# Kernel tuning notes

Measured on AMD Instinct MI355X. Metric: run time of the kernel, lower is better.

Reference implementation:

```python
import jax, jax.numpy as jnp
import numpy as np

# irreps_in = irreps_out = "32x0e + 16x1o"; irreps_edge = "1x0e + 1x1o"
N_SCAL, N_VEC = 32, 16
RADIAL_EMBED, HIDDEN = 64, 64
# FullyConnectedTensorProduct instructions (uvw), v == 1 since edge mults are 1:
#  P1: 0e x 0e -> 0e (32*32)   P2: 1o x 1o -> 0e (16*32)
#  P3: 0e x 1o -> 1o (32*16)   P4: 1o x 0e -> 1o (16*16)   P5: 1o x 1o -> 1o (16*16)
SPLITS = np.cumsum([0, 32 * 32, 16 * 32, 32 * 16, 16 * 16, 16 * 16])
W_NUMEL = int(SPLITS[-1])  # 2560
SILU_NORM = 1.6790425  # e3nn normalize2mom constant for silu
# path weights: alpha = ir_out.dim / sum(num_elements over paths into same output)
PW0 = (1.0 / (32.0 + 16.0)) ** 0.5          # scalar output paths
PW1 = (3.0 / (32.0 + 16.0 + 16.0)) ** 0.5   # vector output paths
INV_SQRT3 = 3.0 ** -0.5  # wigner_3j(0,1,1)/(1,0,1)/(1,1,0) magnitude
INV_SQRT6 = 6.0 ** -0.5  # wigner_3j(1,1,1) = eps_ijk / sqrt(6)
N_NODES, N_EDGES = 8192, 65536


def radial_net(e, W0, W1, W2):
    # e3nn FullyConnectedNet: x @ (W / sqrt(fan_in)), normalized silu between layers
    h = e
    for W in (W0, W1):
        h = jax.nn.silu(h @ (W / jnp.sqrt(jnp.float32(W.shape[0])))) * SILU_NORM
    return h @ (W2 / jnp.sqrt(jnp.float32(W2.shape[0])))


def setup_inputs() -> dict:
    key = jax.random.key(0)
    ks = jax.random.split(key, 9)
    edge_index = jax.random.randint(ks[0], (2, N_EDGES), 0, N_NODES)
    node_feat = jax.random.normal(ks[1], (N_NODES, N_SCAL + 3 * N_VEC), jnp.float32)
    edge_feat = jax.random.normal(ks[2], (N_EDGES, 4), jnp.float32)
    edge_embed = jax.random.normal(ks[3], (N_EDGES, RADIAL_EMBED), jnp.float32)
    W_fc0 = jax.random.normal(ks[4], (RADIAL_EMBED, HIDDEN), jnp.float32)
    W_fc1 = jax.random.normal(ks[5], (HIDDEN, HIDDEN), jnp.float32)
    W_fc2 = jax.random.normal(ks[6], (HIDDEN, W_NUMEL), jnp.float32)
    Wsc0 = jax.random.normal(ks[7], (N_SCAL, N_SCAL), jnp.float32)
    Wsc1 = jax.random.normal(ks[8], (N_VEC, N_VEC), jnp.float32)
    return dict(edge_index=edge_index, node_feat=node_feat, edge_feat=edge_feat,
                edge_embed=edge_embed, dim_size=N_NODES,
                W_fc0=W_fc0, W_fc1=W_fc1, W_fc2=W_fc2, Wsc0=Wsc0, Wsc1=Wsc1)


def reference(edge_index, node_feat, edge_feat, edge_embed, dim_size,
              W_fc0, W_fc1, W_fc2, Wsc0, Wsc1):
    src, dst = edge_index[0], edge_index[1]
    w = radial_net(edge_embed, W_fc0, W_fc1, W_fc2)  # [E, 2560]
    W1 = w[:, SPLITS[0]:SPLITS[1]].reshape(-1, 32, 32)
    W2 = w[:, SPLITS[1]:SPLITS[2]].reshape(-1, 16, 32)
    W3 = w[:, SPLITS[2]:SPLITS[3]].reshape(-1, 32, 16)
    W4 = w[:, SPLITS[3]:SPLITS[4]].reshape(-1, 16, 16)
    W5 = w[:, SPLITS[4]:SPLITS[5]].reshape(-1, 16, 16)
    xe = node_feat[src]                                    # gather [E, 80]
    x0 = xe[:, :N_SCAL]                                    # [E, 32]
    x1 = xe[:, N_SCAL:].reshape(-1, N_VEC, 3)              # [E, 16, 3]
    y0, y1 = edge_feat[:, 0], edge_feat[:, 1:4]            # [E], [E, 3]
    # scalar outputs
    dot = jnp.einsum('eui,ei->eu', x1, y1)
    out0 = PW0 * (jnp.einsum('euw,eu,e->ew', W1, x0, y0)
                  + INV_SQRT3 * jnp.einsum('euw,eu->ew', W2, dot))
    # vector outputs ((x cross y)_k = eps_ijk x_i y_j)
    cross = jnp.cross(x1, y1[:, None, :])
    out1 = PW1 * (INV_SQRT3 * jnp.einsum('euw,eu,ek->ewk', W3, x0, y1)
                  + INV_SQRT3 * jnp.einsum('euw,euk,e->ewk', W4, x1, y0)
                  + INV_SQRT6 * jnp.einsum('euw,euk->ewk', W5, cross))
    msg = jnp.concatenate([out0, out1.reshape(-1, 3 * N_VEC)], axis=1)  # [E, 80]
    agg = jax.ops.segment_sum(msg, dst, num_segments=dim_size)          # [N, 80]
    # self-connection: e3nn o3.Linear applied per irrep, / sqrt(fan_in)
    n0 = node_feat[:, :N_SCAL]
    n1 = node_feat[:, N_SCAL:].reshape(-1, N_VEC, 3)
    sc0 = n0 @ Wsc0 / jnp.sqrt(jnp.float32(N_SCAL))
    sc1 = jnp.einsum('nui,uv->nvi', n1, Wsc1) / jnp.sqrt(jnp.float32(N_VEC))
    sc = jnp.concatenate([sc0, sc1.reshape(-1, 3 * N_VEC)], axis=1)
    return agg + sc
```

## Files before the change

kernel.cpp:

```cpp
#include <hip/hip_runtime.h>

typedef unsigned short u16;
typedef __bf16 bf16x8 __attribute__((ext_vector_type(8)));
typedef float  f32x4  __attribute__((ext_vector_type(4)));

#define NEDGES 65536
#define NNODES 8192
#define EPB 64

#define PW0f       0.14433756729740643f
#define PW1f       0.21650635094610965f
#define INV_SQRT3f 0.5773502691896258f
#define INV_SQRT6f 0.4082482904638631f
#define SILU_NORMf 1.6790425f

#define WT2_OFF 0
#define WT0_OFF 163840
#define WT1_OFF 167936
#define WS_ELEMS 172032

#define OFF_CNT   344064
#define OFF_OFS   376832
#define OFF_CUR   409856
#define OFF_ELIST 442624
#define OFF_MSG   704768
#define WS_NEED   21676288

#define HSTR 72

__device__ __forceinline__ float silu_n(float z) {
    return SILU_NORMf * z / (1.0f + __expf(-z));
}
__device__ __forceinline__ u16 f2bf(float f) {
    return __builtin_bit_cast(u16, (__bf16)f);
}
__device__ __forceinline__ float bf2f(u16 u) {
    unsigned v = ((unsigned)u) << 16;
    return __builtin_bit_cast(float, v);
}
__device__ __forceinline__ bf16x8 ld_bf8(const u16* p) {
    return *reinterpret_cast<const bf16x8*>(p);
}
__device__ __forceinline__ bf16x8 cvt_bf8(const float* p) {
    float4 a = *reinterpret_cast<const float4*>(p);
    float4 b = *reinterpret_cast<const float4*>(p + 4);
    bf16x8 r;
    r[0]=(__bf16)a.x; r[1]=(__bf16)a.y; r[2]=(__bf16)a.z; r[3]=(__bf16)a.w;
    r[4]=(__bf16)b.x; r[5]=(__bf16)b.y; r[6]=(__bf16)b.z; r[7]=(__bf16)b.w;
    return r;
}
#define MFMA16(A,B,C) __builtin_amdgcn_mfma_f32_16x16x32_bf16(A,B,C,0,0,0)

__global__ void k_zero(int* __restrict__ cnt) {
    int i = blockIdx.x * 256 + threadIdx.x;
    if (i < NNODES) cnt[i] = 0;
}

__global__ void k_prep(const float* __restrict__ Wfc0,
                       const float* __restrict__ Wfc1,
                       const float* __restrict__ Wfc2,
                       const float* __restrict__ node_feat,
                       const float* __restrict__ Wsc0,
                       const float* __restrict__ Wsc1,
                       const int*   __restrict__ eidx,
                       u16* __restrict__ ws,
                       int* __restrict__ cnt,
                       float* __restrict__ out)
{
    const int bid = blockIdx.x;
    if (bid < 672) {
        int gid = bid * 256 + threadIdx.x;
        if (gid < 163840) {
            int k = gid / 2560;
            int j = gid - k * 2560;
            float s;
            if (j < 1024)      s = PW0f;
            else if (j < 1536) s = PW0f * INV_SQRT3f;
            else if (j < 2304) s = PW1f * INV_SQRT3f;
            else               s = PW1f * INV_SQRT6f;
            ws[WT2_OFF + j * 64 + k] = f2bf(Wfc2[gid] * (0.125f * s));
        } else if (gid < WT1_OFF) {
            int i = gid - WT0_OFF;
            int k = i >> 6, n = i & 63;
            ws[WT0_OFF + n * 64 + k] = f2bf(Wfc0[i] * 0.125f);
        } else if (gid < WS_ELEMS) {
            int i = gid - WT1_OFF;
            int k = i >> 6, n = i & 63;
            ws[WT1_OFF + n * 64 + k] = f2bf(Wfc1[i] * 0.125f);
        }
    } else if (bid < 3232) {
        int gid = (bid - 672) * 256 + threadIdx.x;
        if (gid >= NNODES * 80) return;
        int n = gid / 80;
        int s = gid - n * 80;
        const float* nf = node_feat + (size_t)n * 80;
        float r;
        if (s < 32) {
            float a = 0.f;
            #pragma unroll
            for (int u = 0; u < 32; ++u) a += nf[u] * Wsc0[u * 32 + s];
            r = a * 0.17677669529663687f;
        } else {
            int v = (s - 32) / 3;
            int k = (s - 32) - v * 3;
            float a = 0.f;
            #pragma unroll
            for (int u = 0; u < 16; ++u) a += nf[32 + u * 3 + k] * Wsc1[u * 16 + v];
            r = a * 0.25f;
        }
        out[gid] = r;
    } else {
        int e = (bid - 3232) * 256 + threadIdx.x;
        if (e < NEDGES) atomicAdd(&cnt[eidx[NEDGES + e]], 1);
    }
}

__global__ __launch_bounds__(1024) void k_scan(const int* __restrict__ cnt,
                                               int* __restrict__ ofs,
                                               int* __restrict__ cur)
{
    __shared__ int ps[1024];
    const int t = threadIdx.x;
    const int base = t * 8;
    int v[8]; int s = 0;
    #pragma unroll
    for (int i = 0; i < 8; ++i) { v[i] = cnt[base + i]; s += v[i]; }
    ps[t] = s;
    __syncthreads();
    int acc = s;
    for (int off = 1; off < 1024; off <<= 1) {
        int x = (t >= off) ? ps[t - off] : 0;
        __syncthreads();
        acc += x;
        ps[t] = acc;
        __syncthreads();
    }
    int run = acc - s;
    #pragma unroll
    for (int i = 0; i < 8; ++i) { ofs[base + i] = run; cur[base + i] = run; run += v[i]; }
    if (t == 1023) ofs[NNODES] = run;
}

__global__ void k_fill(const int* __restrict__ eidx,
                       int* __restrict__ cur,
                       int* __restrict__ elist)
{
    int e = blockIdx.x * 256 + threadIdx.x;
    int d = eidx[NEDGES + e];
    int pos = atomicAdd(&cur[d], 1);
    elist[pos] = e;
}

template<int TAIL>
__global__ __launch_bounds__(256, 3) void k_main(
    const int*   __restrict__ eidx,
    const float* __restrict__ node_feat,
    const float* __restrict__ edge_feat,
    const float* __restrict__ edge_embed,
    const u16*   __restrict__ ws,
    float*       __restrict__ msgbuf,
    float*       __restrict__ out)
{
    __shared__ __align__(16) char smem[40192];
    u16*   h1S   = (u16*)(smem);
    u16*   c12S  = (u16*)(smem + 9216);
    u16*   coefB = (u16*)(smem + 15360);
    int*   dstS  = (int*)(smem + 39936);
    u16*   h0S   = (u16*)(smem + 15360);
    float* msgS  = (float*)(smem + 9216);

    const int t    = threadIdx.x;
    const int lane = t & 63;
    const int l15  = lane & 15;
    const int lq   = lane >> 4;
    const int wid  = t >> 6;
    const int role = (wid + blockIdx.x) & 3;
    const int eg0  = blockIdx.x * EPB;

    const u16* WT2 = ws + WT2_OFF;
    const u16* WT0 = ws + WT0_OFF;
    const u16* WT1 = ws + WT1_OFF;

    {
        const float* erow = edge_embed + (size_t)(eg0 + wid * 16 + l15) * 64 + 8 * lq;
        bf16x8 eB0 = cvt_bf8(erow);
        bf16x8 eB1 = cvt_bf8(erow + 32);
        #pragma unroll
        for (int ntl = 0; ntl < 4; ++ntl) {
            const u16* a = WT0 + (ntl * 16 + l15) * 64 + 8 * lq;
            bf16x8 A0 = ld_bf8(a);
            bf16x8 A1 = ld_bf8(a + 32);
            f32x4 z = {0.f, 0.f, 0.f, 0.f};
            z = MFMA16(A0, eB0, z);
            f32x4 dd = MFMA16(A1, eB1, z);
            ushort4 pk;
            pk.x = f2bf(silu_n(dd[0]));
            pk.y = f2bf(silu_n(dd[1]));
            pk.z = f2bf(silu_n(dd[2]));
            pk.w = f2bf(silu_n(dd[3]));
            *(ushort4*)&h0S[(wid * 16 + l15) * HSTR + ntl * 16 + lq * 4] = pk;
        }
    }
    {
        const u16* hrow = h0S + (wid * 16 + l15) * HSTR + 8 * lq;
        bf16x8 hB0 = ld_bf8(hrow);
        bf16x8 hB1 = ld_bf8(hrow + 32);
        #pragma unroll
        for (int ntl = 0; ntl < 4; ++ntl) {
            const u16* a = WT1 + (ntl * 16 + l15) * 64 + 8 * lq;
            bf16x8 A0 = ld_bf8(a);
            bf16x8 A1 = ld_bf8(a + 32);
            f32x4 z = {0.f, 0.f, 0.f, 0.f};
            z = MFMA16(A0, hB0, z);
            f32x4 dd = MFMA16(A1, hB1, z);
            ushort4 pk;
            pk.x = f2bf(silu_n(dd[0]));
            pk.y = f2bf(silu_n(dd[1]));
            pk.z = f2bf(silu_n(dd[2]));
            pk.w = f2bf(silu_n(dd[3]));
            *(ushort4*)&h1S[(wid * 16 + l15) * HSTR + ntl * 16 + lq * 4] = pk;
        }
    }
    __syncthreads();

    {
        const int e   = t & 63;
        const int q   = t >> 6;
        const int eg  = eg0 + e;
        const int src = eidx[eg];
        const float* nf = node_feat + (size_t)src * 80;
        const float* ef = edge_feat + (size_t)eg * 4;
        if (q == 0) {
            dstS[e] = eidx[NEDGES + eg];
            const float y0 = ef[0];
            #pragma unroll
            for (int u = 0; u < 32; ++u) c12S[u * 64 + e] = f2bf(nf[u] * y0);
        } else if (q == 1) {
            const float ya = ef[1], yb = ef[2], yc = ef[3];
            #pragma unroll
            for (int u = 0; u < 16; ++u) {
                float d = nf[32 + u * 3] * ya + nf[32 + u * 3 + 1] * yb
                        + nf[32 + u * 3 + 2] * yc;
                c12S[(32 + u) * 64 + e] = f2bf(d);
            }
        } else if (q == 2) {
            const float ya = ef[1], yb = ef[2], yc = ef[3];
            #pragma unroll
            for (int u = 0; u < 32; ++u) {
                const float x = nf[u];
                coefB[(u * 3 + 0) * 64 + e] = f2bf(x * ya);
                coefB[(u * 3 + 1) * 64 + e] = f2bf(x * yb);
                coefB[(u * 3 + 2) * 64 + e] = f2bf(x * yc);
            }
        } else {
            const float y0 = ef[0], ya = ef[1], yb = ef[2], yc = ef[3];
            #pragma unroll
            for (int u = 0; u < 16; ++u) {
                const float xa = nf[32 + u * 3], xb = nf[32 + u * 3 + 1], xc = nf[32 + u * 3 + 2];
                coefB[(96 + u * 3 + 0) * 64 + e] = f2bf(xa * y0);
                coefB[(96 + u * 3 + 1) * 64 + e] = f2bf(xb * y0);
                coefB[(96 + u * 3 + 2) * 64 + e] = f2bf(xc * y0);
                coefB[(144 + u * 3 + 0) * 64 + e] = f2bf(xb * yc - xc * yb);
                coefB[(144 + u * 3 + 1) * 64 + e] = f2bf(xc * ya - xa * yc);
                coefB[(144 + u * 3 + 2) * 64 + e] = f2bf(xa * yb - xb * ya);
            }
        }
    }
    __syncthreads();

    bf16x8 hb[4][2];
    #pragma unroll
    for (int eg = 0; eg < 4; ++eg) {
        const u16* r = h1S + (eg * 16 + l15) * HSTR + 8 * lq;
        hb[eg][0] = ld_bf8(r);
        hb[eg][1] = ld_bf8(r + 32);
    }

    float acc[48];
    #pragma unroll
    for (int i = 0; i < 48; ++i) acc[i] = 0.f;

    int t0, ntile;
    if (role < 2) { t0 = role * 48;            ntile = 48; }
    else          { t0 = 96 + (role - 2) * 32; ntile = 32; }

    const u16* Aw = WT2 + l15 * 64 + 8 * lq;

#define COMPUTE(A0_, A1_, D_)                                          \
    {                                                                  \
        _Pragma("unroll")                                              \
        for (int eg = 0; eg < 4; ++eg) {                               \
            f32x4 z = {0.f, 0.f, 0.f, 0.f};                            \
            z = MFMA16(A0_, hb[eg][0], z);                             \
            D_[eg] = MFMA16(A1_, hb[eg][1], z);                        \
        }                                                              \
    }

#define EPILOGUE(D_, TT_, HS_)                                              \
    {                                                                       \
        if (role < 2) {                                                     \
            const u16* cr = c12S + ((TT_) >> 1) * 64;                       \
            _Pragma("unroll")                                               \
            for (int eg = 0; eg < 4; ++eg) {                                \
                const float c = bf2f(cr[eg * 16 + l15]);                    \
                _Pragma("unroll")                                           \
                for (int r = 0; r < 4; ++r)                                 \
                    acc[eg * 8 + (HS_) * 4 + r] += c * D_[eg][r];           \
            }                                                               \
        } else {                                                            \
            const u16* cr = coefB + ((TT_) - 96) * 192;                     \
            _Pragma("unroll")                                               \
            for (int eg = 0; eg < 4; ++eg) {                                \
                const int e16 = eg * 16 + l15;                              \
                const float c0 = bf2f(cr[e16]);                             \
                const float c1 = bf2f(cr[64 + e16]);                        \
                const float c2 = bf2f(cr[128 + e16]);                       \
                _Pragma("unroll")                                           \
                for (int r = 0; r < 4; ++r) {                               \
                    const float dv = D_[eg][r];                             \
                    acc[eg * 12 + r * 3 + 0] += c0 * dv;                    \
                    acc[eg * 12 + r * 3 + 1] += c1 * dv;                    \
                    acc[eg * 12 + r * 3 + 2] += c2 * dv;                    \
                }                                                           \
            }                                                               \
        }                                                                   \
    }

    bf16x8 Pa0, Pa1, Pb0, Pb1, Qa0, Qa1, Qb0, Qb1;
    {
        const u16* p0 = Aw + (size_t)(t0 + 0) * 1024;
        Pa0 = ld_bf8(p0); Pa1 = ld_bf8(p0 + 32);
        const u16* p1 = Aw + (size_t)(t0 + 1) * 1024;
        Pb0 = ld_bf8(p1); Pb1 = ld_bf8(p1 + 32);
        const u16* p2 = Aw + (size_t)(t0 + 2) * 1024;
        Qa0 = ld_bf8(p2); Qa1 = ld_bf8(p2 + 32);
        const u16* p3 = Aw + (size_t)(t0 + 3) * 1024;
        Qb0 = ld_bf8(p3); Qb1 = ld_bf8(p3 + 32);
    }
    const int nq = ntile >> 2;
    #pragma unroll 1
    for (int p = 0; p < nq; ++p) {
        const int tt = t0 + 4 * p;
        const bool more = (p + 1 < nq);
        f32x4 d[4];
        COMPUTE(Pa0, Pa1, d);
        EPILOGUE(d, tt, 0);
        if (more) { const u16* q_ = Aw + (size_t)(tt + 4) * 1024;
                    Pa0 = ld_bf8(q_); Pa1 = ld_bf8(q_ + 32); }
        COMPUTE(Pb0, Pb1, d);
        EPILOGUE(d, tt + 1, 1);
        if (more) { const u16* q_ = Aw + (size_t)(tt + 5) * 1024;
                    Pb0 = ld_bf8(q_); Pb1 = ld_bf8(q_ + 32); }
        COMPUTE(Qa0, Qa1, d);
        EPILOGUE(d, tt + 2, 0);
        if (more) { const u16* q_ = Aw + (size_t)(tt + 6) * 1024;
                    Qa0 = ld_bf8(q_); Qa1 = ld_bf8(q_ + 32); }
        COMPUTE(Qb0, Qb1, d);
        EPILOGUE(d, tt + 3, 1);
        if (more) { const u16* q_ = Aw + (size_t)(tt + 7) * 1024;
                    Qb0 = ld_bf8(q_); Qb1 = ld_bf8(q_ + 32); }
    }
#undef COMPUTE
#undef EPILOGUE

    __syncthreads();
    if (role == 0) {
        #pragma unroll
        for (int eg = 0; eg < 4; ++eg) {
            float* mb = msgS + (eg * 16 + l15) * 81;
            #pragma unroll
            for (int hs = 0; hs < 2; ++hs)
                #pragma unroll
                for (int r = 0; r < 4; ++r)
                    mb[hs * 16 + lq * 4 + r] = acc[eg * 8 + hs * 4 + r];
        }
    } else if (role == 2) {
        #pragma unroll
        for (int eg = 0; eg < 4; ++eg) {
            float* mb = msgS + (eg * 16 + l15) * 81 + 32;
            #pragma unroll
            for (int r = 0; r < 4; ++r)
                #pragma unroll
                for (int k = 0; k < 3; ++k)
                    mb[(lq * 4 + r) * 3 + k] = acc[eg * 12 + r * 3 + k];
        }
    }
    __syncthreads();
    if (role == 1) {
        #pragma unroll
        for (int eg = 0; eg < 4; ++eg) {
            float* mb = msgS + (eg * 16 + l15) * 81;
            #pragma unroll
            for (int hs = 0; hs < 2; ++hs)
                #pragma unroll
                for (int r = 0; r < 4; ++r)
                    mb[hs * 16 + lq * 4 + r] += acc[eg * 8 + hs * 4 + r];
        }
    } else if (role == 3) {
        #pragma unroll
        for (int eg = 0; eg < 4; ++eg) {
            float* mb = msgS + (eg * 16 + l15) * 81 + 32;
            #pragma unroll
            for (int r = 0; r < 4; ++r)
                #pragma unroll
                for (int k = 0; k < 3; ++k)
                    mb[(lq * 4 + r) * 3 + k] += acc[eg * 12 + r * 3 + k];
        }
    }
    __syncthreads();

    if (TAIL == 1) {
        float* mrow = msgbuf + (size_t)eg0 * 80;
        for (int idx = t; idx < EPB * 80; idx += 256) {
            const int e = idx / 80;
            const int s = idx - e * 80;
            mrow[idx] = msgS[e * 81 + s];
        }
    } else {
        for (int idx = t; idx < 64 * 81; idx += 256) {
            const int e = idx / 81;
            const int s = idx - e * 81;
            if (s < 80)
                atomicAdd(out + (size_t)dstS[e] * 80 + s, msgS[idx]);
        }
    }
}

__global__ __launch_bounds__(256) void k_gather(const int* __restrict__ ofs,
                                                const int* __restrict__ elist,
                                                const float* __restrict__ msg,
                                                float* __restrict__ out)
{
    const int lane = threadIdx.x & 63;
    const int n = blockIdx.x * 4 + (threadIdx.x >> 6);
    const int jb = ofs[n], je = ofs[n + 1];
    float v0 = 0.f, v1 = 0.f;
    int j = jb;
    for (; j + 2 <= je; j += 2) {
        const int e0 = elist[j], e1 = elist[j + 1];
        const float* m0 = msg + (size_t)e0 * 80;
        const float* m1 = msg + (size_t)e1 * 80;
        v0 += m0[lane] + m1[lane];
        if (lane < 16) v1 += m0[64 + lane] + m1[64 + lane];
    }
    if (j < je) {
        const float* m0 = msg + (size_t)elist[j] * 80;
        v0 += m0[lane];
        if (lane < 16) v1 += m0[64 + lane];
    }
    float* op = out + (size_t)n * 80;
    op[lane] += v0;
    if (lane < 16) op[64 + lane] += v1;
}

extern "C" void kernel_launch(void* const* d_in, const int* in_sizes, int n_in,
                              void* d_out, int out_size, void* d_ws, size_t ws_size,
                              hipStream_t stream) {
    const int*   eidx       = (const int*)d_in[0];
    const float* node_feat  = (const float*)d_in[1];
    const float* edge_feat  = (const float*)d_in[2];
    const float* edge_embed = (const float*)d_in[3];
    const float* Wfc0       = (const float*)d_in[5];
    const float* Wfc1       = (const float*)d_in[6];
    const float* Wfc2       = (const float*)d_in[7];
    const float* Wsc0       = (const float*)d_in[8];
    const float* Wsc1       = (const float*)d_in[9];
    float* out = (float*)d_out;
    char*  wsb = (char*)d_ws;
    u16*   ws  = (u16*)d_ws;

    if (ws_size < (size_t)WS_ELEMS * sizeof(u16)) return;

    const bool big = ws_size >= (size_t)WS_NEED;
    int*   cnt    = (int*)(wsb + OFF_CNT);
    int*   ofs    = (int*)(wsb + OFF_OFS);
    int*   cur    = (int*)(wsb + OFF_CUR);
    int*   elist  = (int*)(wsb + OFF_ELIST);
    float* msgbuf = (float*)(wsb + OFF_MSG);

    if (big) {
        hipLaunchKernelGGL(k_zero, dim3(32), dim3(256), 0, stream, cnt);
        hipLaunchKernelGGL(k_prep, dim3(3488), dim3(256), 0, stream,
                           Wfc0, Wfc1, Wfc2, node_feat, Wsc0, Wsc1, eidx, ws, cnt, out);
        hipLaunchKernelGGL(k_scan, dim3(1), dim3(1024), 0, stream, cnt, ofs, cur);
        hipLaunchKernelGGL(k_fill, dim3(NEDGES / 256), dim3(256), 0, stream,
                           eidx, cur, elist);
        hipLaunchKernelGGL((k_main<1>), dim3(NEDGES / EPB), dim3(256), 0, stream,
                           eidx, node_feat, edge_feat, edge_embed, ws, msgbuf, out);
        hipLaunchKernelGGL(k_gather, dim3(NNODES / 4), dim3(256), 0, stream,
                           ofs, elist, msgbuf, out);
    } else {
        hipLaunchKernelGGL(k_prep, dim3(3232), dim3(256), 0, stream,
                           Wfc0, Wfc1, Wfc2, node_feat, Wsc0, Wsc1, eidx, ws, cnt, out);
        hipLaunchKernelGGL((k_main<0>), dim3(NEDGES / EPB), dim3(256), 0, stream,
                           eidx, node_feat, edge_feat, edge_embed, ws, msgbuf, out);
    }
}
```

Before: 101.9 us.

## Factor P3 path as scalar contraction times y1 and rebalance wave roles

The P3 path (0e x 1o -> 1o) is now computed as a contraction of W3 against x0 alone, with the result multiplied by y1 after accumulation. This replaces per-component coefficients (x0*ya, x0*yb, x0*yc) with a single scalar coefficient. The remaining vector coefficients are stored packed as ushort4 per edge, and the tile ranges per wave role are rebalanced (44/44/40/32). The change adds an extra LDS merge pass with a barrier and drops launch bounds occupancy from 3 to 2 blocks, which may change register allocation and latency hiding.

```diff
diff --git a/kernel.cpp b/kernel.cpp
--- a/kernel.cpp
+++ b/kernel.cpp
@@ -152,7 +152,7 @@
 }
 
 template<int TAIL>
-__global__ __launch_bounds__(256, 3) void k_main(
+__global__ __launch_bounds__(256, 2) void k_main(
     const int*   __restrict__ eidx,
     const float* __restrict__ node_feat,
     const float* __restrict__ edge_feat,
@@ -161,13 +161,16 @@
     float*       __restrict__ msgbuf,
     float*       __restrict__ out)
 {
-    __shared__ __align__(16) char smem[40192];
-    u16*   h1S   = (u16*)(smem);
-    u16*   c12S  = (u16*)(smem + 9216);
-    u16*   coefB = (u16*)(smem + 15360);
-    int*   dstS  = (int*)(smem + 39936);
-    u16*   h0S   = (u16*)(smem + 15360);
-    float* msgS  = (float*)(smem + 9216);
+    __shared__ __align__(16) char smem[36864];
+    u16*   h1S  = (u16*)(smem);
+    u16*   c12S = (u16*)(smem + 9216);
+    u16*   x0S  = (u16*)(smem + 15360);
+    u16*   w4S  = (u16*)(smem + 19456);
+    u16*   w5S  = (u16*)(smem + 27648);
+    float* y1S  = (float*)(smem + 35840);
+    int*   dstS = (int*)(smem + 36608);
+    u16*   h0S  = (u16*)(smem + 9216);
+    float* msgS = (float*)(smem + 9216);
 
     const int t    = threadIdx.x;
     const int lane = t & 63;
@@ -233,6 +236,7 @@
         if (q == 0) {
             dstS[e] = eidx[NEDGES + eg];
             const float y0 = ef[0];
+            y1S[e] = ef[1]; y1S[64 + e] = ef[2]; y1S[128 + e] = ef[3];
             #pragma unroll
             for (int u = 0; u < 32; ++u) c12S[u * 64 + e] = f2bf(nf[u] * y0);
         } else if (q == 1) {
@@ -243,26 +247,30 @@
                         + nf[32 + u * 3 + 2] * yc;
                 c12S[(32 + u) * 64 + e] = f2bf(d);
             }
+            #pragma unroll
+            for (int u = 0; u < 32; ++u) x0S[u * 64 + e] = f2bf(nf[u]);
         } else if (q == 2) {
-            const float ya = ef[1], yb = ef[2], yc = ef[3];
-            #pragma unroll
-            for (int u = 0; u < 32; ++u) {
-                const float x = nf[u];
-                coefB[(u * 3 + 0) * 64 + e] = f2bf(x * ya);
-                coefB[(u * 3 + 1) * 64 + e] = f2bf(x * yb);
-                coefB[(u * 3 + 2) * 64 + e] = f2bf(x * yc);
+            const float y0 = ef[0];
+            #pragma unroll
+            for (int u = 0; u < 16; ++u) {
+                ushort4 pk;
+                pk.x = f2bf(nf[32 + u * 3 + 0] * y0);
+                pk.y = f2bf(nf[32 + u * 3 + 1] * y0);
+                pk.z = f2bf(nf[32 + u * 3 + 2] * y0);
+                pk.w = 0;
+                *(ushort4*)&w4S[(u * 64 + e) * 4] = pk;
             }
         } else {
-            const float y0 = ef[0], ya = ef[1], yb = ef[2], yc = ef[3];
+            const float ya = ef[1], yb = ef[2], yc = ef[3];
             #pragma unroll
             for (int u = 0; u < 16; ++u) {
                 const float xa = nf[32 + u * 3], xb = nf[32 + u * 3 + 1], xc = nf[32 + u * 3 + 2];
-                coefB[(96 + u * 3 + 0) * 64 + e] = f2bf(xa * y0);
-                coefB[(96 + u * 3 + 1) * 64 + e] = f2bf(xb * y0);
-                coefB[(96 + u * 3 + 2) * 64 + e] = f2bf(xc * y0);
-                coefB[(144 + u * 3 + 0) * 64 + e] = f2bf(xb * yc - xc * yb);
-                coefB[(144 + u * 3 + 1) * 64 + e] = f2bf(xc * ya - xa * yc);
-                coefB[(144 + u * 3 + 2) * 64 + e] = f2bf(xa * yb - xb * ya);
+                ushort4 pk;
+                pk.x = f2bf(xb * yc - xc * yb);
+                pk.y = f2bf(xc * ya - xa * yc);
+                pk.z = f2bf(xa * yb - xb * ya);
+                pk.w = 0;
+                *(ushort4*)&w5S[(u * 64 + e) * 4] = pk;
             }
         }
     }
@@ -281,8 +289,10 @@
     for (int i = 0; i < 48; ++i) acc[i] = 0.f;
 
     int t0, ntile;
-    if (role < 2) { t0 = role * 48;            ntile = 48; }
-    else          { t0 = 96 + (role - 2) * 32; ntile = 32; }
+    if      (role == 0) { t0 = 0;   ntile = 44; }
+    else if (role == 1) { t0 = 44;  ntile = 44; }
+    else if (role == 2) { t0 = 88;  ntile = 40; }
+    else                { t0 = 128; ntile = 32; }
 
     const u16* Aw = WT2 + l15 * 64 + 8 * lq;
 
@@ -296,34 +306,44 @@
         }                                                              \
     }
 
-#define EPILOGUE(D_, TT_, HS_)                                              \
-    {                                                                       \
-        if (role < 2) {                                                     \
-            const u16* cr = c12S + ((TT_) >> 1) * 64;                       \
-            _Pragma("unroll")                                               \
-            for (int eg = 0; eg < 4; ++eg) {                                \
-                const float c = bf2f(cr[eg * 16 + l15]);                    \
-                _Pragma("unroll")                                           \
-                for (int r = 0; r < 4; ++r)                                 \
-                    acc[eg * 8 + (HS_) * 4 + r] += c * D_[eg][r];           \
-            }                                                               \
-        } else {                                                            \
-            const u16* cr = coefB + ((TT_) - 96) * 192;                     \
-            _Pragma("unroll")                                               \
-            for (int eg = 0; eg < 4; ++eg) {                                \
-                const int e16 = eg * 16 + l15;                              \
-                const float c0 = bf2f(cr[e16]);                             \
-                const float c1 = bf2f(cr[64 + e16]);                        \
-                const float c2 = bf2f(cr[128 + e16]);                       \
-                _Pragma("unroll")                                           \
-                for (int r = 0; r < 4; ++r) {                               \
-                    const float dv = D_[eg][r];                             \
-                    acc[eg * 12 + r * 3 + 0] += c0 * dv;                    \
-                    acc[eg * 12 + r * 3 + 1] += c1 * dv;                    \
-                    acc[eg * 12 + r * 3 + 2] += c2 * dv;                    \
-                }                                                           \
-            }                                                               \
-        }                                                                   \
+#define EPILOGUE(D_, TT_, HS_)                                               \
+    {                                                                        \
+        if ((TT_) < 96) {                         \
+            const u16* cr = c12S + ((TT_) >> 1) * 64;                        \
+            _Pragma("unroll")                                                \
+            for (int eg = 0; eg < 4; ++eg) {                                 \
+                const float c = bf2f(cr[eg * 16 + l15]);                     \
+                _Pragma("unroll")                                            \
+                for (int r = 0; r < 4; ++r)                                  \
+                    acc[eg * 8 + (HS_) * 4 + r] += c * D_[eg][r];            \
+            }                                                                \
+        } else if ((TT_) < 128) {             \
+            const u16* cr = x0S + ((TT_) - 96) * 64;                         \
+            _Pragma("unroll")                                                \
+            for (int eg = 0; eg < 4; ++eg) {                                 \
+                const float c = bf2f(cr[eg * 16 + l15]);                     \
+                _Pragma("unroll")                                            \
+                for (int r = 0; r < 4; ++r)                                  \
+                    acc[32 + eg * 4 + r] += c * D_[eg][r];                   \
+            }                                                                \
+        } else {                                   \
+            const u16* cr = ((TT_) < 144 ? w4S + ((TT_) - 128) * 256         \
+                                         : w5S + ((TT_) - 144) * 256);       \
+            _Pragma("unroll")                                                \
+            for (int eg = 0; eg < 4; ++eg) {                                 \
+                const ushort4 cw = *(const ushort4*)&cr[(eg * 16 + l15) * 4];\
+                const float c0 = bf2f(cw.x);                                 \
+                const float c1 = bf2f(cw.y);                                 \
+                const float c2 = bf2f(cw.z);                                 \
+                _Pragma("unroll")                                            \
+                for (int r = 0; r < 4; ++r) {                                \
+                    const float dv = D_[eg][r];                              \
+                    acc[eg * 12 + r * 3 + 0] += c0 * dv;                     \
+                    acc[eg * 12 + r * 3 + 1] += c1 * dv;                     \
+                    acc[eg * 12 + r * 3 + 2] += c2 * dv;                     \
+                }                                                            \
+            }                                                                \
+        }                                                                    \
     }
 
     bf16x8 Pa0, Pa1, Pb0, Pb1, Qa0, Qa1, Qb0, Qb1;
@@ -374,7 +394,7 @@
                 for (int r = 0; r < 4; ++r)
                     mb[hs * 16 + lq * 4 + r] = acc[eg * 8 + hs * 4 + r];
         }
-    } else if (role == 2) {
+    } else if (role == 3) {
         #pragma unroll
         for (int eg = 0; eg < 4; ++eg) {
             float* mb = msgS + (eg * 16 + l15) * 81 + 32;
@@ -396,15 +416,31 @@
                 for (int r = 0; r < 4; ++r)
                     mb[hs * 16 + lq * 4 + r] += acc[eg * 8 + hs * 4 + r];
         }
-    } else if (role == 3) {
+    } else if (role == 2) {
         #pragma unroll
         for (int eg = 0; eg < 4; ++eg) {
-            float* mb = msgS + (eg * 16 + l15) * 81 + 32;
-            #pragma unroll
-            for (int r = 0; r < 4; ++r)
+            const int e = eg * 16 + l15;
+            const float w1x = y1S[e], w1y = y1S[64 + e], w1z = y1S[128 + e];
+            float* mb = msgS + e * 81 + 32;
+            #pragma unroll
+            for (int r = 0; r < 4; ++r) {
+                const float s = acc[32 + eg * 4 + r];
+                mb[(lq * 4 + r) * 3 + 0] += s * w1x;
+                mb[(lq * 4 + r) * 3 + 1] += s * w1y;
+                mb[(lq * 4 + r) * 3 + 2] += s * w1z;
+            }
+        }
+    }
+    __syncthreads();
+    if (role == 2) {
+        #pragma unroll
+        for (int eg = 0; eg < 4; ++eg) {
+            float* mb = msgS + (eg * 16 + l15) * 81;
+            #pragma unroll
+            for (int hs = 0; hs < 2; ++hs)
                 #pragma unroll
-                for (int k = 0; k < 3; ++k)
-                    mb[(lq * 4 + r) * 3 + k] += acc[eg * 12 + r * 3 + k];
+                for (int r = 0; r < 4; ++r)
+                    mb[hs * 16 + lq * 4 + r] += acc[eg * 8 + hs * 4 + r];
         }
     }
     __syncthreads();
```

Measured after the change: 101.0 us. About the same (-0.9%).
